# Optimization experiments

Hardware: AMD Instinct MI355X
Metric: run time of the kernel (lower is better)

Reference implementation:

```python
import jax, jax.numpy as jnp
import numpy as np

N = 50000      # nodes
E = 800000     # edges
IN = 128       # in_dim
H = 128        # hidden_dim
OUT = 64       # out_dim
B = 6          # block_num
NEG_SLOPE = 0.01  # nn.LeakyReLU default


def setup_inputs() -> dict:
    key = jax.random.key(0)
    ks = jax.random.split(key, 10)
    s = 0.05
    return {
        "inputs": jax.random.normal(ks[0], (N, IN), jnp.float32),
        "edges": jax.random.randint(ks[1], (2, E), 0, N, jnp.int32),
        "w_in": jax.random.normal(ks[2], (IN, H), jnp.float32) * s,
        "b_in": jnp.zeros((H,), jnp.float32),
        "w1": jax.random.normal(ks[3], (B, H, H), jnp.float32) * s,
        "b1": jnp.zeros((B, H), jnp.float32),
        "w2": jax.random.normal(ks[4], (B, H, H), jnp.float32) * s,
        "b2": jnp.zeros((B, H), jnp.float32),
        "w_out": jax.random.normal(ks[5], (H, OUT), jnp.float32) * s,
        "b_out": jnp.zeros((OUT,), jnp.float32),
    }


def _leaky(x):
    return jnp.where(x >= 0, x, NEG_SLOPE * x)


def _gcn_conv(x, W, b, src, dst, norm):
    # GCNConv: out = D^{-1/2}(A+I)D^{-1/2} (x W) + b, with self-loops folded in.
    xw = x @ W                                   # [N, d_out]
    msg = xw[src] * norm[src, None]              # gather + edge scaling [E, d_out]
    agg = jax.ops.segment_sum(msg, dst, num_segments=N)
    agg = agg * norm[:, None] + xw * (norm * norm)[:, None]  # neighbors + self-loop
    return agg + b


def reference(inputs, edges, w_in, b_in, w1, b1, w2, b2, w_out, b_out):
    src, dst = edges[0], edges[1]
    deg = 1.0 + jax.ops.segment_sum(jnp.ones((E,), inputs.dtype), dst, num_segments=N)
    norm = jax.lax.rsqrt(deg)                    # [N]

    x = _leaky(_gcn_conv(inputs, w_in, b_in, src, dst, norm))
    for i in range(B):  # fixed small layer loop (structurally distinct params)
        h = _leaky(_gcn_conv(x, w1[i], b1[i], src, dst, norm))
        h = _leaky(_gcn_conv(h, w2[i], b2[i], src, dst, norm))
        x = (x + h) * 0.5
    # dropout in eval mode -> identity
    x_out = _gcn_conv(x, w_out, b_out, src, dst, norm)
    return (x_out, x)
```

## Files before the change

### kernel.cpp

```cpp
#include <hip/hip_runtime.h>

#define NNODES 50000
#define NPAD   50048
#define NEDGES 800000
#define HDIM 128
#define OUTDIM 64

#define GEMM_GRID 391
#define GEMM_BLK  512
#define GEMM_TILES (NPAD / 16)

typedef short short8 __attribute__((ext_vector_type(8)));
typedef _Float16 half8 __attribute__((ext_vector_type(8)));
typedef _Float16 half4 __attribute__((ext_vector_type(4)));
typedef float f32x4 __attribute__((ext_vector_type(4)));
typedef float f32x8 __attribute__((ext_vector_type(8)));

__device__ __forceinline__ unsigned short f2bf(float f) {
    unsigned int u = __builtin_bit_cast(unsigned int, f);
    unsigned int r = (u + 0x7FFFu + ((u >> 16) & 1u)) >> 16;
    return (unsigned short)r;
}
__device__ __forceinline__ float bf2f(unsigned short b) {
    unsigned int u = ((unsigned int)b) << 16;
    return __builtin_bit_cast(float, u);
}

__global__ void count_kernel(const int* __restrict__ dst, int* __restrict__ deg,
                             int* __restrict__ epos) {
    int e = blockIdx.x * 256 + threadIdx.x;
    if (e < NEDGES) epos[e] = atomicAdd(&deg[dst[e]], 1);
}

__global__ __launch_bounds__(256) void bsum_kernel(const int* __restrict__ deg,
                                                   int* __restrict__ bsum) {
    __shared__ int red[256];
    int i = blockIdx.x * 256 + threadIdx.x;
    red[threadIdx.x] = (i < NNODES) ? deg[i] : 0;
    __syncthreads();
    for (int off = 128; off; off >>= 1) {
        if (threadIdx.x < off) red[threadIdx.x] += red[threadIdx.x + off];
        __syncthreads();
    }
    if (threadIdx.x == 0) bsum[blockIdx.x] = red[0];
}

__global__ __launch_bounds__(256) void bscan_kernel(const int* __restrict__ bsum,
                                                    int* __restrict__ bofs) {
    __shared__ int s[256];
    int t = threadIdx.x;
    int v = (t < 196) ? bsum[t] : 0;
    s[t] = v;
    __syncthreads();
    for (int off = 1; off < 256; off <<= 1) {
        int u = (t >= off) ? s[t - off] : 0;
        __syncthreads();
        s[t] += u;
        __syncthreads();
    }
    if (t < 196) bofs[t] = s[t] - v;
}

__global__ __launch_bounds__(256) void emit_kernel(
    const int* __restrict__ deg, const int* __restrict__ bofs,
    int* __restrict__ row_ptr, float* __restrict__ norm) {
    __shared__ int s[256];
    int t = threadIdx.x;
    int i = blockIdx.x * 256 + t;
    int v = (i < NNODES) ? deg[i] : 0;
    s[t] = v;
    __syncthreads();
    for (int off = 1; off < 256; off <<= 1) {
        int u = (t >= off) ? s[t - off] : 0;
        __syncthreads();
        s[t] += u;
        __syncthreads();
    }
    int excl = s[t] - v + bofs[blockIdx.x];
    if (i < NNODES) {
        row_ptr[i] = excl;
        norm[i] = rsqrtf(1.0f + (float)v);
    }
    if (i == NNODES - 1) row_ptr[NNODES] = NEDGES;
}

__global__ void fill_kernel(const int* __restrict__ src, const int* __restrict__ dst,
                            const int* __restrict__ epos, const int* __restrict__ row_ptr,
                            int* __restrict__ sorted_src) {
    int e = blockIdx.x * 256 + threadIdx.x;
    if (e < NEDGES) sorted_src[row_ptr[dst[e]] + epos[e]] = src[e];
}

__global__ __launch_bounds__(256) void prep_w_kernel(
    const float* __restrict__ w_in, const float* __restrict__ w1,
    const float* __restrict__ w2, const float* __restrict__ w_out,
    unsigned short* __restrict__ wT, _Float16* __restrict__ w2f) {
    int idx = blockIdx.x * 256 + threadIdx.x;
    if (idx < 16384 + 98304) {
        const float* W;
        unsigned short* o;
        int e;
        if (idx < 16384) {
            W = w_in; o = wT; e = idx;
        } else {
            int j = idx - 16384; int m = j >> 14; e = j & 16383;
            W = w1 + ((size_t)m << 14); o = wT + (size_t)(1 + m) * 32768;
        }
        int k = e >> 7, n = e & 127;
        float v = W[e];
        unsigned short h = f2bf(v);
        o[(size_t)n * 256 + k] = h;
        o[(size_t)n * 256 + 128 + k] = f2bf(v - bf2f(h));
    } else if (idx < 16384 + 196608) {
        int j = idx - 16384 - 98304; int m = j >> 14; int e = j & 16383;
        int k = e >> 7, n = e & 127;
        w2f[(size_t)m * 16384 + n * 128 + k] = (_Float16)w2[((size_t)m << 14) + e];
    } else {
        int e = idx - 212992;
        int k = e >> 6, n = e & 63;
        float v = w_out[e];
        unsigned short h = f2bf(v);
        unsigned short* o = wT + (size_t)7 * 32768;
        o[(size_t)n * 256 + k] = h;
        o[(size_t)n * 256 + 128 + k] = f2bf(v - bf2f(h));
    }
}

__global__ __launch_bounds__(256) void split_x_kernel(
    const float* __restrict__ x, unsigned short* __restrict__ xc) {
    int gid = blockIdx.x * 256 + threadIdx.x;
    int row = gid >> 6;
    int kk = (gid & 63) * 2;
    float2 v = {0.f, 0.f};
    if (row < NNODES) v = *(const float2*)(x + (size_t)row * 128 + kk);
    unsigned short h0 = f2bf(v.x), h1 = f2bf(v.y);
    unsigned short l0 = f2bf(v.x - bf2f(h0)), l1 = f2bf(v.y - bf2f(h1));
    *(unsigned int*)(xc + (size_t)row * 256 + kk) =
        (unsigned int)h0 | ((unsigned int)h1 << 16);
    *(unsigned int*)(xc + (size_t)row * 256 + 128 + kk) =
        (unsigned int)l0 | ((unsigned int)l1 << 16);
}

template <int NCOLS>
__global__ __launch_bounds__(GEMM_BLK) void gemm_bf_kernel(
    const unsigned short* __restrict__ xc, const unsigned short* __restrict__ wT,
    const float* __restrict__ norm, _Float16* __restrict__ y) {
    __shared__ unsigned short Blds[NCOLS * 256];
    const int t = threadIdx.x;
    const int wave = t >> 6, lane = t & 63, quad = lane >> 4, l16 = lane & 15;

    constexpr int NCH = NCOLS * 32;
#pragma unroll
    for (int i = 0; i < NCH / GEMM_BLK; ++i) {
        int C = i * GEMM_BLK + t;
        int n = C >> 5, c = C & 31;
        const unsigned short* gp = wT + ((size_t)n << 8) + ((c ^ (n & 7)) << 3);
        unsigned short* lp = Blds + ((size_t)C << 3);
        __builtin_amdgcn_global_load_lds(
            (const __attribute__((address_space(1))) void*)gp,
            (__attribute__((address_space(3))) void*)lp, 16, 0, 0);
    }
    __syncthreads();

    const int wid = blockIdx.x * (GEMM_BLK / 64) + wave;
    const int sw = l16 & 7;
    const int rb0 = wid * 16;

    short8 a0[8];
    const unsigned short* ap0 = xc + ((size_t)(rb0 + l16) << 8) + quad * 8;
#pragma unroll
    for (int ck = 0; ck < 8; ++ck) a0[ck] = *(const short8*)(ap0 + ck * 32);

    float nm0[4];
#pragma unroll
    for (int r = 0; r < 4; ++r) {
        int r0 = rb0 + quad * 4 + r;
        nm0[r] = norm[r0 < NNODES ? r0 : 0];
    }

#pragma unroll
    for (int nt = 0; nt < NCOLS / 16; ++nt) {
        const unsigned short* bp = Blds + ((size_t)(nt * 16 + l16) << 8);
        short8 bh[4], bl[4];
#pragma unroll
        for (int ck = 0; ck < 4; ++ck) {
            bh[ck] = *(const short8*)(bp + (((ck * 4 + quad) ^ sw) << 3));
            bl[ck] = *(const short8*)(bp + (((16 + ck * 4 + quad) ^ sw) << 3));
        }
        f32x4 ac0 = (f32x4){0.f, 0.f, 0.f, 0.f};
#pragma unroll
        for (int ck = 0; ck < 4; ++ck) {
            ac0 = __builtin_amdgcn_mfma_f32_16x16x32_bf16(a0[ck], bh[ck], ac0, 0, 0, 0);
            ac0 = __builtin_amdgcn_mfma_f32_16x16x32_bf16(a0[ck], bl[ck], ac0, 0, 0, 0);
            ac0 = __builtin_amdgcn_mfma_f32_16x16x32_bf16(a0[4 + ck], bh[ck], ac0, 0, 0, 0);
        }
        int col = nt * 16 + l16;
#pragma unroll
        for (int r = 0; r < 4; ++r) {
            int r0 = rb0 + quad * 4 + r;
            if (r0 < NNODES) y[(size_t)r0 * NCOLS + col] = (_Float16)(ac0[r] * nm0[r]);
        }
    }
}

__global__ __launch_bounds__(GEMM_BLK) void gemm_f16_kernel(
    const _Float16* __restrict__ A, const _Float16* __restrict__ wf,
    const float* __restrict__ norm, _Float16* __restrict__ y) {
    __shared__ _Float16 Blds[128 * 128];
    const int t = threadIdx.x;
    const int wave = t >> 6, lane = t & 63, quad = lane >> 4, l16 = lane & 15;

#pragma unroll
    for (int i = 0; i < 2048 / GEMM_BLK; ++i) {
        int C = i * GEMM_BLK + t;
        int n = C >> 4, c = C & 15;
        const _Float16* gp = wf + ((size_t)n << 7) + ((c ^ (n & 7)) << 3);
        _Float16* lp = Blds + ((size_t)C << 3);
        __builtin_amdgcn_global_load_lds(
            (const __attribute__((address_space(1))) void*)gp,
            (__attribute__((address_space(3))) void*)lp, 16, 0, 0);
    }
    __syncthreads();

    const int wid = blockIdx.x * (GEMM_BLK / 64) + wave;
    const int sw = l16 & 7;
    const int rb0 = wid * 16;

    half8 a0[4];
    const _Float16* ap0 = A + ((size_t)(rb0 + l16) << 7) + quad * 8;
#pragma unroll
    for (int ck = 0; ck < 4; ++ck) a0[ck] = *(const half8*)(ap0 + ck * 32);

    float nm0[4];
#pragma unroll
    for (int r = 0; r < 4; ++r) {
        int r0 = rb0 + quad * 4 + r;
        nm0[r] = norm[r0 < NNODES ? r0 : 0];
    }

#pragma unroll
    for (int nt = 0; nt < 8; ++nt) {
        const _Float16* bp = Blds + ((size_t)(nt * 16 + l16) << 7);
        half8 b[4];
#pragma unroll
        for (int ck = 0; ck < 4; ++ck)
            b[ck] = *(const half8*)(bp + (((ck * 4 + quad) ^ sw) << 3));
        f32x4 ac0 = (f32x4){0.f, 0.f, 0.f, 0.f};
#pragma unroll
        for (int ck = 0; ck < 4; ++ck)
            ac0 = __builtin_amdgcn_mfma_f32_16x16x32_f16(a0[ck], b[ck], ac0, 0, 0, 0);
        int col = nt * 16 + l16;
#pragma unroll
        for (int r = 0; r < 4; ++r) {
            int r0 = rb0 + quad * 4 + r;
            if (r0 < NNODES) y[(size_t)r0 * 128 + col] = (_Float16)(ac0[r] * nm0[r]);
        }
    }
}

template <int MODE, bool WOUT, bool OUT16>
__global__ __launch_bounds__(256) void gather_fin128(
    const _Float16* __restrict__ y, const int* __restrict__ row_ptr,
    const int* __restrict__ sorted_src, const float* __restrict__ norm,
    const float* __restrict__ bias, const unsigned short* __restrict__ xcres,
    float* __restrict__ out, unsigned short* __restrict__ xcout,
    _Float16* __restrict__ h16) {
    const int wave = threadIdx.x >> 6;
    const int lane = threadIdx.x & 63;
    const int g = lane >> 4, j = lane & 15;
    const int n = blockIdx.x * 16 + wave * 4 + g;
    const int beg = row_ptr[n];
    const int deg = row_ptr[n + 1] - beg;
    int dmax = deg;
    dmax = max(dmax, __shfl_xor(dmax, 16));
    dmax = max(dmax, __shfl_xor(dmax, 32));

    f32x8 acc = (f32x8){0.f, 0.f, 0.f, 0.f, 0.f, 0.f, 0.f, 0.f};

    for (int i = 0; i < dmax; i += 8) {
        int sarr[8];
#pragma unroll
        for (int u = 0; u < 8; ++u)
            sarr[u] = (i + u < deg) ? sorted_src[beg + i + u] : -1;
        half8 h[8];
#pragma unroll
        for (int u = 0; u < 8; ++u)
            if (sarr[u] >= 0)
                h[u] = *(const half8*)(y + ((size_t)sarr[u] << 7) + j * 8);
#pragma unroll
        for (int u = 0; u < 8; ++u)
            if (sarr[u] >= 0) acc += __builtin_convertvector(h[u], f32x8);
    }

    const half8 sh = *(const half8*)(y + ((size_t)n << 7) + j * 8);
    const f32x4 b0 = *(const f32x4*)(bias + j * 8);
    const f32x4 b1 = *(const f32x4*)(bias + j * 8 + 4);
    const float bb[8] = {b0[0], b0[1], b0[2], b0[3], b1[0], b1[1], b1[2], b1[3]};
    const float nm = norm[n];
    float v[8];
#pragma unroll
    for (int c = 0; c < 8; ++c) {
        float t = (acc[c] + (float)sh[c]) * nm + bb[c];
        v[c] = t >= 0.f ? t : 0.01f * t;
    }
    if (MODE == 1) {
        short8 hw = __builtin_nontemporal_load(
            (const short8*)(xcres + ((size_t)n << 8) + j * 8));
        short8 lw = __builtin_nontemporal_load(
            (const short8*)(xcres + ((size_t)n << 8) + 128 + j * 8));
#pragma unroll
        for (int c = 0; c < 8; ++c) {
            float xr = bf2f((unsigned short)hw[c]) + bf2f((unsigned short)lw[c]);
            v[c] = (xr + v[c]) * 0.5f;
        }
    }
    if (WOUT) {
        f32x4 o0 = (f32x4){v[0], v[1], v[2], v[3]};
        f32x4 o1 = (f32x4){v[4], v[5], v[6], v[7]};
        __builtin_nontemporal_store(o0, (f32x4*)(out + ((size_t)n << 7) + j * 8));
        __builtin_nontemporal_store(o1, (f32x4*)(out + ((size_t)n << 7) + j * 8 + 4));
    }
    if (OUT16) {
        half8 o;
#pragma unroll
        for (int c = 0; c < 8; ++c) o[c] = (_Float16)v[c];
        *(half8*)(h16 + ((size_t)n << 7) + j * 8) = o;
    } else {
        short8 hi, lo;
#pragma unroll
        for (int c = 0; c < 8; ++c) {
            unsigned short hv = f2bf(v[c]);
            hi[c] = (short)hv;
            lo[c] = (short)f2bf(v[c] - bf2f(hv));
        }
        *(short8*)(xcout + ((size_t)n << 8) + j * 8) = hi;
        *(short8*)(xcout + ((size_t)n << 8) + 128 + j * 8) = lo;
    }
}

__global__ __launch_bounds__(256) void gather_fin64(
    const _Float16* __restrict__ y, const int* __restrict__ row_ptr,
    const int* __restrict__ sorted_src, const float* __restrict__ norm,
    const float* __restrict__ bias, float* __restrict__ out) {
    const int wave = threadIdx.x >> 6;
    const int lane = threadIdx.x & 63;
    const int g = lane >> 4, j = lane & 15;
    const int n = blockIdx.x * 16 + wave * 4 + g;
    const int beg = row_ptr[n];
    const int deg = row_ptr[n + 1] - beg;
    int dmax = deg;
    dmax = max(dmax, __shfl_xor(dmax, 16));
    dmax = max(dmax, __shfl_xor(dmax, 32));

    f32x4 acc = (f32x4){0.f, 0.f, 0.f, 0.f};
    for (int i = 0; i < dmax; i += 8) {
        int sarr[8];
#pragma unroll
        for (int u = 0; u < 8; ++u)
            sarr[u] = (i + u < deg) ? sorted_src[beg + i + u] : -1;
        half4 h[8];
#pragma unroll
        for (int u = 0; u < 8; ++u)
            if (sarr[u] >= 0)
                h[u] = *(const half4*)(y + ((size_t)sarr[u] << 6) + j * 4);
#pragma unroll
        for (int u = 0; u < 8; ++u)
            if (sarr[u] >= 0) acc += __builtin_convertvector(h[u], f32x4);
    }

    const half4 sh = *(const half4*)(y + ((size_t)n << 6) + j * 4);
    const f32x4 b = *(const f32x4*)(bias + j * 4);
    const float nm = norm[n];
    f32x4 o;
    o[0] = (acc[0] + (float)sh[0]) * nm + b[0];
    o[1] = (acc[1] + (float)sh[1]) * nm + b[1];
    o[2] = (acc[2] + (float)sh[2]) * nm + b[2];
    o[3] = (acc[3] + (float)sh[3]) * nm + b[3];
    __builtin_nontemporal_store(o, (f32x4*)(out + ((size_t)n << 6) + j * 4));
}

extern "C" void kernel_launch(void* const* d_in, const int* in_sizes, int n_in,
                              void* d_out, int out_size, void* d_ws, size_t ws_size,
                              hipStream_t stream) {
    const float* inputs = (const float*)d_in[0];
    const int* edges = (const int*)d_in[1];
    const int* src = edges;
    const int* dst = edges + NEDGES;
    const float* w_in  = (const float*)d_in[2];
    const float* b_in  = (const float*)d_in[3];
    const float* w1    = (const float*)d_in[4];
    const float* b1    = (const float*)d_in[5];
    const float* w2    = (const float*)d_in[6];
    const float* b2    = (const float*)d_in[7];
    const float* w_out = (const float*)d_in[8];
    const float* b_out = (const float*)d_in[9];

    float* out  = (float*)d_out;
    float* xout = out;
    float* x    = out + (size_t)NNODES * OUTDIM;

    char* p = (char*)d_ws;
    auto alloc = [&](size_t bytes) {
        char* r = p;
        p += (bytes + 63) & ~(size_t)63;
        return r;
    };
    int* deg        = (int*)alloc(NNODES * 4);
    int* epos       = (int*)alloc(NEDGES * 4);
    int* row_ptr    = (int*)alloc((NNODES + 1) * 4);
    int* bsum       = (int*)alloc(256 * 4);
    int* bofs       = (int*)alloc(256 * 4);
    int* sorted_src = (int*)alloc(NEDGES * 4);
    float* normb    = (float*)alloc(NNODES * 4);
    unsigned short* wT = (unsigned short*)alloc((size_t)245760 * 2);
    _Float16* w2f   = (_Float16*)alloc((size_t)6 * 16384 * 2);
    unsigned short* xc_x = (unsigned short*)alloc((size_t)NPAD * 256 * 2);
    unsigned short* xc_in = (unsigned short*)alloc((size_t)NPAD * 256 * 2);
    _Float16* h16   = (_Float16*)alloc((size_t)NPAD * 128 * 2);
    _Float16* y     = (_Float16*)alloc((size_t)NNODES * HDIM * 2);

    hipMemsetAsync(deg, 0, NNODES * sizeof(int), stream);
    count_kernel<<<(NEDGES + 255) / 256, 256, 0, stream>>>(dst, deg, epos);
    bsum_kernel<<<196, 256, 0, stream>>>(deg, bsum);
    bscan_kernel<<<1, 256, 0, stream>>>(bsum, bofs);
    emit_kernel<<<196, 256, 0, stream>>>(deg, bofs, row_ptr, normb);
    fill_kernel<<<(NEDGES + 255) / 256, 256, 0, stream>>>(src, dst, epos, row_ptr, sorted_src);
    prep_w_kernel<<<864, 256, 0, stream>>>(w_in, w1, w2, w_out, wT, w2f);

    split_x_kernel<<<(NPAD * 64) / 256, 256, 0, stream>>>(inputs, xc_in);
    gemm_bf_kernel<128><<<GEMM_GRID, GEMM_BLK, 0, stream>>>(xc_in, wT, normb, y);
    gather_fin128<0, false, false><<<NNODES / 16, 256, 0, stream>>>(
        y, row_ptr, sorted_src, normb, b_in, nullptr, nullptr, xc_x, nullptr);

    for (int i = 0; i < 6; ++i) {
        gemm_bf_kernel<128><<<GEMM_GRID, GEMM_BLK, 0, stream>>>(
            xc_x, wT + (size_t)(1 + i) * 32768, normb, y);
        gather_fin128<0, false, true><<<NNODES / 16, 256, 0, stream>>>(
            y, row_ptr, sorted_src, normb, b1 + i * HDIM, nullptr, nullptr, nullptr, h16);
        gemm_f16_kernel<<<GEMM_GRID, GEMM_BLK, 0, stream>>>(
            h16, w2f + (size_t)i * 16384, normb, y);
        if (i < 5)
            gather_fin128<1, false, false><<<NNODES / 16, 256, 0, stream>>>(
                y, row_ptr, sorted_src, normb, b2 + i * HDIM, xc_x, nullptr, xc_x, nullptr);
        else
            gather_fin128<1, true, false><<<NNODES / 16, 256, 0, stream>>>(
                y, row_ptr, sorted_src, normb, b2 + i * HDIM, xc_x, x, xc_x, nullptr);
    }

    gemm_bf_kernel<64><<<GEMM_GRID, GEMM_BLK, 0, stream>>>(
        xc_x, wT + (size_t)7 * 32768, normb, y);
    gather_fin64<<<NNODES / 16, 256, 0, stream>>>(
        y, row_ptr, sorted_src, normb, b_out, xout);
}
```

Before: 784.4 us.

## Fuse first-conv gather/finalize into second GEMM via LDS staging

Merges the gather-aggregate-finalize kernel of the first block conv into the following f16 GEMM. Each wave gathers neighbor rows for its 16 nodes, applies norm, bias and LeakyReLU, and stages the f16 result in LDS as the MFMA A operand. This removes the h16 round trip through global memory and one kernel launch per block, and writes the GEMM output to a separate buffer y2 so it does not overwrite y while other blocks still read it. In exchange, gather parallelism is reduced (391 blocks of 512 threads instead of 3125 blocks), LDS use grows by 32KB per block, and the gather latency now serializes ahead of the MFMA work.

Result: faster. 742.6 us (-5.3%).

```diff
diff --git a/kernel.cpp b/kernel.cpp
--- a/kernel.cpp
+++ b/kernel.cpp
@@ -203,10 +203,13 @@
     }
 }
 
-__global__ __launch_bounds__(GEMM_BLK) void gemm_f16_kernel(
-    const _Float16* __restrict__ A, const _Float16* __restrict__ wf,
-    const float* __restrict__ norm, _Float16* __restrict__ y) {
+__global__ __launch_bounds__(GEMM_BLK) void fgg_f16_kernel(
+    const _Float16* __restrict__ y, const int* __restrict__ row_ptr,
+    const int* __restrict__ sorted_src, const float* __restrict__ norm,
+    const float* __restrict__ bias, const _Float16* __restrict__ wf,
+    _Float16* __restrict__ yout) {
     __shared__ _Float16 Blds[128 * 128];
+    __shared__ _Float16 Alds[8 * 16 * 128];
     const int t = threadIdx.x;
     const int wave = t >> 6, lane = t & 63, quad = lane >> 4, l16 = lane & 15;
 
@@ -220,16 +223,63 @@
             (const __attribute__((address_space(1))) void*)gp,
             (__attribute__((address_space(3))) void*)lp, 16, 0, 0);
     }
+
+    const int wid = blockIdx.x * (GEMM_BLK / 64) + wave;
+    const int rb0 = wid * 16;
+    _Float16* Aw = Alds + (size_t)wave * 2048;
+    const int g = quad, j = l16;
+
+    for (int tb = 0; tb < 4; ++tb) {
+        const int n = rb0 + tb * 4 + g;
+        const bool valid = n < NNODES;
+        const int beg = valid ? row_ptr[n] : 0;
+        const int dg = valid ? (row_ptr[n + 1] - beg) : 0;
+        int dmax = dg;
+        dmax = max(dmax, __shfl_xor(dmax, 16));
+        dmax = max(dmax, __shfl_xor(dmax, 32));
+
+        f32x8 acc = (f32x8){0.f, 0.f, 0.f, 0.f, 0.f, 0.f, 0.f, 0.f};
+        for (int i = 0; i < dmax; i += 8) {
+            int sarr[8];
+#pragma unroll
+            for (int u = 0; u < 8; ++u)
+                sarr[u] = (i + u < dg) ? sorted_src[beg + i + u] : -1;
+            half8 h[8];
+#pragma unroll
+            for (int u = 0; u < 8; ++u)
+                if (sarr[u] >= 0)
+                    h[u] = *(const half8*)(y + ((size_t)sarr[u] << 7) + j * 8);
+#pragma unroll
+            for (int u = 0; u < 8; ++u)
+                if (sarr[u] >= 0) acc += __builtin_convertvector(h[u], f32x8);
+        }
+
+        half8 o;
+        if (valid) {
+            const half8 sh = *(const half8*)(y + ((size_t)n << 7) + j * 8);
+            const f32x4 b0 = *(const f32x4*)(bias + j * 8);
+            const f32x4 b1 = *(const f32x4*)(bias + j * 8 + 4);
+            const float bb[8] = {b0[0], b0[1], b0[2], b0[3], b1[0], b1[1], b1[2], b1[3]};
+            const float nm = norm[n];
+#pragma unroll
+            for (int c = 0; c < 8; ++c) {
+                float v = (acc[c] + (float)sh[c]) * nm + bb[c];
+                v = v >= 0.f ? v : 0.01f * v;
+                o[c] = (_Float16)v;
+            }
+        } else {
+#pragma unroll
+            for (int c = 0; c < 8; ++c) o[c] = (_Float16)0.f;
+        }
+        *(half8*)(Aw + (size_t)(tb * 4 + g) * 128 + j * 8) = o;
+    }
     __syncthreads();
 
-    const int wid = blockIdx.x * (GEMM_BLK / 64) + wave;
     const int sw = l16 & 7;
-    const int rb0 = wid * 16;
-
     half8 a0[4];
-    const _Float16* ap0 = A + ((size_t)(rb0 + l16) << 7) + quad * 8;
-#pragma unroll
-    for (int ck = 0; ck < 4; ++ck) a0[ck] = *(const half8*)(ap0 + ck * 32);
+#pragma unroll
+    for (int ck = 0; ck < 4; ++ck)
+        a0[ck] = *(const half8*)(Aw + (size_t)l16 * 128 + ck * 32 + quad * 8);
 
     float nm0[4];
 #pragma unroll
@@ -253,7 +303,7 @@
 #pragma unroll
         for (int r = 0; r < 4; ++r) {
             int r0 = rb0 + quad * 4 + r;
-            if (r0 < NNODES) y[(size_t)r0 * 128 + col] = (_Float16)(ac0[r] * nm0[r]);
+            if (r0 < NNODES) yout[(size_t)r0 * 128 + col] = (_Float16)(ac0[r] * nm0[r]);
         }
     }
 }
@@ -416,7 +466,7 @@
     _Float16* w2f   = (_Float16*)alloc((size_t)6 * 16384 * 2);
     unsigned short* xc_x = (unsigned short*)alloc((size_t)NPAD * 256 * 2);
     unsigned short* xc_in = (unsigned short*)alloc((size_t)NPAD * 256 * 2);
-    _Float16* h16   = (_Float16*)alloc((size_t)NPAD * 128 * 2);
+    _Float16* y2    = (_Float16*)alloc((size_t)NPAD * 128 * 2);
     _Float16* y     = (_Float16*)alloc((size_t)NNODES * HDIM * 2);
 
     hipMemsetAsync(deg, 0, NNODES * sizeof(int), stream);
@@ -435,16 +485,15 @@
     for (int i = 0; i < 6; ++i) {
         gemm_bf_kernel<128><<<GEMM_GRID, GEMM_BLK, 0, stream>>>(
             xc_x, wT + (size_t)(1 + i) * 32768, normb, y);
-        gather_fin128<0, false, true><<<NNODES / 16, 256, 0, stream>>>(
-            y, row_ptr, sorted_src, normb, b1 + i * HDIM, nullptr, nullptr, nullptr, h16);
-        gemm_f16_kernel<<<GEMM_GRID, GEMM_BLK, 0, stream>>>(
-            h16, w2f + (size_t)i * 16384, normb, y);
+        fgg_f16_kernel<<<GEMM_GRID, GEMM_BLK, 0, stream>>>(
+            y, row_ptr, sorted_src, normb, b1 + i * HDIM,
+            w2f + (size_t)i * 16384, y2);
         if (i < 5)
             gather_fin128<1, false, false><<<NNODES / 16, 256, 0, stream>>>(
-                y, row_ptr, sorted_src, normb, b2 + i * HDIM, xc_x, nullptr, xc_x, nullptr);
+                y2, row_ptr, sorted_src, normb, b2 + i * HDIM, xc_x, nullptr, xc_x, nullptr);
         else
             gather_fin128<1, true, false><<<NNODES / 16, 256, 0, stream>>>(
-                y, row_ptr, sorted_src, normb, b2 + i * HDIM, xc_x, x, xc_x, nullptr);
+                y2, row_ptr, sorted_src, normb, b2 + i * HDIM, xc_x, x, xc_x, nullptr);
     }
 
     gemm_bf_kernel<64><<<GEMM_GRID, GEMM_BLK, 0, stream>>>(
```

## Fuse gather-aggregate epilogue with next layer's GEMM and use f16 weights

Applied to the files above, without the earlier changes.

Each gather/finalize step now feeds its output rows straight into LDS and runs the following layer's f16 MFMA GEMM in the same kernel, removing the intermediate activation round trip and roughly halving kernel launches. The w1 and w_out GEMMs switch from split-bf16 (three MFMAs per step) to single f16 MFMAs, cutting GEMM work but lowering precision. Ping-pong y buffers are used so no kernel reads a buffer it is writing. The gather part now runs with 512-thread blocks across 391 blocks, which changes occupancy and latency hiding for the irregular gather.

Result: faster. 706.6 us (-9.9%).

```diff
diff --git a/kernel.cpp b/kernel.cpp
--- a/kernel.cpp
+++ b/kernel.cpp
@@ -8,7 +8,6 @@
 
 #define GEMM_GRID 391
 #define GEMM_BLK  512
-#define GEMM_TILES (NPAD / 16)
 
 typedef short short8 __attribute__((ext_vector_type(8)));
 typedef _Float16 half8 __attribute__((ext_vector_type(8)));
@@ -94,23 +93,20 @@
 __global__ __launch_bounds__(256) void prep_w_kernel(
     const float* __restrict__ w_in, const float* __restrict__ w1,
     const float* __restrict__ w2, const float* __restrict__ w_out,
-    unsigned short* __restrict__ wT, _Float16* __restrict__ w2f) {
+    unsigned short* __restrict__ wT, _Float16* __restrict__ w1f,
+    _Float16* __restrict__ w2f, _Float16* __restrict__ woutf) {
     int idx = blockIdx.x * 256 + threadIdx.x;
-    if (idx < 16384 + 98304) {
-        const float* W;
-        unsigned short* o;
-        int e;
-        if (idx < 16384) {
-            W = w_in; o = wT; e = idx;
-        } else {
-            int j = idx - 16384; int m = j >> 14; e = j & 16383;
-            W = w1 + ((size_t)m << 14); o = wT + (size_t)(1 + m) * 32768;
-        }
+    if (idx < 16384) {
+        int e = idx;
         int k = e >> 7, n = e & 127;
-        float v = W[e];
+        float v = w_in[e];
         unsigned short h = f2bf(v);
-        o[(size_t)n * 256 + k] = h;
-        o[(size_t)n * 256 + 128 + k] = f2bf(v - bf2f(h));
+        wT[(size_t)n * 256 + k] = h;
+        wT[(size_t)n * 256 + 128 + k] = f2bf(v - bf2f(h));
+    } else if (idx < 16384 + 98304) {
+        int j = idx - 16384; int m = j >> 14; int e = j & 16383;
+        int k = e >> 7, n = e & 127;
+        w1f[(size_t)m * 16384 + n * 128 + k] = (_Float16)w1[((size_t)m << 14) + e];
     } else if (idx < 16384 + 196608) {
         int j = idx - 16384 - 98304; int m = j >> 14; int e = j & 16383;
         int k = e >> 7, n = e & 127;
@@ -118,11 +114,7 @@
     } else {
         int e = idx - 212992;
         int k = e >> 6, n = e & 63;
-        float v = w_out[e];
-        unsigned short h = f2bf(v);
-        unsigned short* o = wT + (size_t)7 * 32768;
-        o[(size_t)n * 256 + k] = h;
-        o[(size_t)n * 256 + 128 + k] = f2bf(v - bf2f(h));
+        woutf[(size_t)n * 128 + k] = (_Float16)w_out[e];
     }
 }
 
@@ -203,15 +195,20 @@
     }
 }
 
-__global__ __launch_bounds__(GEMM_BLK) void gemm_f16_kernel(
-    const _Float16* __restrict__ A, const _Float16* __restrict__ wf,
-    const float* __restrict__ norm, _Float16* __restrict__ y) {
-    __shared__ _Float16 Blds[128 * 128];
+template <int MODE, int NCOLS, bool WRXC, bool WOUT>
+__global__ __launch_bounds__(GEMM_BLK) void fga_kernel(
+    const _Float16* __restrict__ y, const int* __restrict__ row_ptr,
+    const int* __restrict__ sorted_src, const float* __restrict__ norm,
+    const float* __restrict__ bias, const unsigned short* __restrict__ xcres,
+    const _Float16* __restrict__ wf, unsigned short* __restrict__ xcout,
+    float* __restrict__ xfull, _Float16* __restrict__ yout) {
+    __shared__ _Float16 Blds[NCOLS * 128];
+    __shared__ _Float16 Alds[8 * 16 * 128];
     const int t = threadIdx.x;
     const int wave = t >> 6, lane = t & 63, quad = lane >> 4, l16 = lane & 15;
 
 #pragma unroll
-    for (int i = 0; i < 2048 / GEMM_BLK; ++i) {
+    for (int i = 0; i < (NCOLS * 16) / GEMM_BLK; ++i) {
         int C = i * GEMM_BLK + t;
         int n = C >> 4, c = C & 15;
         const _Float16* gp = wf + ((size_t)n << 7) + ((c ^ (n & 7)) << 3);
@@ -223,13 +220,90 @@
     __syncthreads();
 
     const int wid = blockIdx.x * (GEMM_BLK / 64) + wave;
+    const int rb0 = wid * 16;
+    _Float16* Aw = Alds + (size_t)wave * 2048;
+    const int g = quad, j = l16;
+
+    for (int tb = 0; tb < 4; ++tb) {
+        const int n = rb0 + tb * 4 + g;
+        const bool valid = n < NNODES;
+        const int beg = valid ? row_ptr[n] : 0;
+        const int dg = valid ? (row_ptr[n + 1] - beg) : 0;
+        int dmax = dg;
+        dmax = max(dmax, __shfl_xor(dmax, 16));
+        dmax = max(dmax, __shfl_xor(dmax, 32));
+
+        f32x8 acc = (f32x8){0.f, 0.f, 0.f, 0.f, 0.f, 0.f, 0.f, 0.f};
+        for (int i = 0; i < dmax; i += 8) {
+            int sarr[8];
+#pragma unroll
+            for (int u = 0; u < 8; ++u)
+                sarr[u] = (i + u < dg) ? sorted_src[beg + i + u] : -1;
+            half8 h[8];
+#pragma unroll
+            for (int u = 0; u < 8; ++u)
+                if (sarr[u] >= 0)
+                    h[u] = *(const half8*)(y + ((size_t)sarr[u] << 7) + j * 8);
+#pragma unroll
+            for (int u = 0; u < 8; ++u)
+                if (sarr[u] >= 0) acc += __builtin_convertvector(h[u], f32x8);
+        }
+
+        half8 o;
+        if (valid) {
+            const half8 sh = *(const half8*)(y + ((size_t)n << 7) + j * 8);
+            const f32x4 b0 = *(const f32x4*)(bias + j * 8);
+            const f32x4 b1 = *(const f32x4*)(bias + j * 8 + 4);
+            const float bb[8] = {b0[0], b0[1], b0[2], b0[3], b1[0], b1[1], b1[2], b1[3]};
+            const float nm = norm[n];
+            float v[8];
+#pragma unroll
+            for (int c = 0; c < 8; ++c) {
+                float tv = (acc[c] + (float)sh[c]) * nm + bb[c];
+                v[c] = tv >= 0.f ? tv : 0.01f * tv;
+            }
+            if (MODE == 1) {
+                short8 hw = __builtin_nontemporal_load(
+                    (const short8*)(xcres + ((size_t)n << 8) + j * 8));
+                short8 lw = __builtin_nontemporal_load(
+                    (const short8*)(xcres + ((size_t)n << 8) + 128 + j * 8));
+#pragma unroll
+                for (int c = 0; c < 8; ++c) {
+                    float xr = bf2f((unsigned short)hw[c]) + bf2f((unsigned short)lw[c]);
+                    v[c] = (xr + v[c]) * 0.5f;
+                }
+            }
+            if (WOUT) {
+                f32x4 o0 = (f32x4){v[0], v[1], v[2], v[3]};
+                f32x4 o1 = (f32x4){v[4], v[5], v[6], v[7]};
+                __builtin_nontemporal_store(o0, (f32x4*)(xfull + ((size_t)n << 7) + j * 8));
+                __builtin_nontemporal_store(o1, (f32x4*)(xfull + ((size_t)n << 7) + j * 8 + 4));
+            }
+            if (WRXC) {
+                short8 hi, lo;
+#pragma unroll
+                for (int c = 0; c < 8; ++c) {
+                    unsigned short hv = f2bf(v[c]);
+                    hi[c] = (short)hv;
+                    lo[c] = (short)f2bf(v[c] - bf2f(hv));
+                }
+                *(short8*)(xcout + ((size_t)n << 8) + j * 8) = hi;
+                *(short8*)(xcout + ((size_t)n << 8) + 128 + j * 8) = lo;
+            }
+#pragma unroll
+            for (int c = 0; c < 8; ++c) o[c] = (_Float16)v[c];
+        } else {
+#pragma unroll
+            for (int c = 0; c < 8; ++c) o[c] = (_Float16)0.f;
+        }
+        *(half8*)(Aw + (size_t)(tb * 4 + g) * 128 + j * 8) = o;
+    }
+
     const int sw = l16 & 7;
-    const int rb0 = wid * 16;
-
     half8 a0[4];
-    const _Float16* ap0 = A + ((size_t)(rb0 + l16) << 7) + quad * 8;
-#pragma unroll
-    for (int ck = 0; ck < 4; ++ck) a0[ck] = *(const half8*)(ap0 + ck * 32);
+#pragma unroll
+    for (int ck = 0; ck < 4; ++ck)
+        a0[ck] = *(const half8*)(Aw + (size_t)l16 * 128 + ck * 32 + quad * 8);
 
     float nm0[4];
 #pragma unroll
@@ -239,7 +313,7 @@
     }
 
 #pragma unroll
-    for (int nt = 0; nt < 8; ++nt) {
+    for (int nt = 0; nt < NCOLS / 16; ++nt) {
         const _Float16* bp = Blds + ((size_t)(nt * 16 + l16) << 7);
         half8 b[4];
 #pragma unroll
@@ -253,88 +327,8 @@
 #pragma unroll
         for (int r = 0; r < 4; ++r) {
             int r0 = rb0 + quad * 4 + r;
-            if (r0 < NNODES) y[(size_t)r0 * 128 + col] = (_Float16)(ac0[r] * nm0[r]);
-        }
-    }
-}
-
-template <int MODE, bool WOUT, bool OUT16>
-__global__ __launch_bounds__(256) void gather_fin128(
-    const _Float16* __restrict__ y, const int* __restrict__ row_ptr,
-    const int* __restrict__ sorted_src, const float* __restrict__ norm,
-    const float* __restrict__ bias, const unsigned short* __restrict__ xcres,
-    float* __restrict__ out, unsigned short* __restrict__ xcout,
-    _Float16* __restrict__ h16) {
-    const int wave = threadIdx.x >> 6;
-    const int lane = threadIdx.x & 63;
-    const int g = lane >> 4, j = lane & 15;
-    const int n = blockIdx.x * 16 + wave * 4 + g;
-    const int beg = row_ptr[n];
-    const int deg = row_ptr[n + 1] - beg;
-    int dmax = deg;
-    dmax = max(dmax, __shfl_xor(dmax, 16));
-    dmax = max(dmax, __shfl_xor(dmax, 32));
-
-    f32x8 acc = (f32x8){0.f, 0.f, 0.f, 0.f, 0.f, 0.f, 0.f, 0.f};
-
-    for (int i = 0; i < dmax; i += 8) {
-        int sarr[8];
-#pragma unroll
-        for (int u = 0; u < 8; ++u)
-            sarr[u] = (i + u < deg) ? sorted_src[beg + i + u] : -1;
-        half8 h[8];
-#pragma unroll
-        for (int u = 0; u < 8; ++u)
-            if (sarr[u] >= 0)
-                h[u] = *(const half8*)(y + ((size_t)sarr[u] << 7) + j * 8);
-#pragma unroll
-        for (int u = 0; u < 8; ++u)
-            if (sarr[u] >= 0) acc += __builtin_convertvector(h[u], f32x8);
-    }
-
-    const half8 sh = *(const half8*)(y + ((size_t)n << 7) + j * 8);
-    const f32x4 b0 = *(const f32x4*)(bias + j * 8);
-    const f32x4 b1 = *(const f32x4*)(bias + j * 8 + 4);
-    const float bb[8] = {b0[0], b0[1], b0[2], b0[3], b1[0], b1[1], b1[2], b1[3]};
-    const float nm = norm[n];
-    float v[8];
-#pragma unroll
-    for (int c = 0; c < 8; ++c) {
-        float t = (acc[c] + (float)sh[c]) * nm + bb[c];
-        v[c] = t >= 0.f ? t : 0.01f * t;
-    }
-    if (MODE == 1) {
-        short8 hw = __builtin_nontemporal_load(
-            (const short8*)(xcres + ((size_t)n << 8) + j * 8));
-        short8 lw = __builtin_nontemporal_load(
-            (const short8*)(xcres + ((size_t)n << 8) + 128 + j * 8));
-#pragma unroll
-        for (int c = 0; c < 8; ++c) {
-            float xr = bf2f((unsigned short)hw[c]) + bf2f((unsigned short)lw[c]);
-            v[c] = (xr + v[c]) * 0.5f;
-        }
-    }
-    if (WOUT) {
-        f32x4 o0 = (f32x4){v[0], v[1], v[2], v[3]};
-        f32x4 o1 = (f32x4){v[4], v[5], v[6], v[7]};
-        __builtin_nontemporal_store(o0, (f32x4*)(out + ((size_t)n << 7) + j * 8));
-        __builtin_nontemporal_store(o1, (f32x4*)(out + ((size_t)n << 7) + j * 8 + 4));
-    }
-    if (OUT16) {
-        half8 o;
-#pragma unroll
-        for (int c = 0; c < 8; ++c) o[c] = (_Float16)v[c];
-        *(half8*)(h16 + ((size_t)n << 7) + j * 8) = o;
-    } else {
-        short8 hi, lo;
-#pragma unroll
-        for (int c = 0; c < 8; ++c) {
-            unsigned short hv = f2bf(v[c]);
-            hi[c] = (short)hv;
-            lo[c] = (short)f2bf(v[c] - bf2f(hv));
-        }
-        *(short8*)(xcout + ((size_t)n << 8) + j * 8) = hi;
-        *(short8*)(xcout + ((size_t)n << 8) + 128 + j * 8) = lo;
+            if (r0 < NNODES) yout[(size_t)r0 * NCOLS + col] = (_Float16)(ac0[r] * nm0[r]);
+        }
     }
 }
 
@@ -412,12 +406,14 @@
     int* bofs       = (int*)alloc(256 * 4);
     int* sorted_src = (int*)alloc(NEDGES * 4);
     float* normb    = (float*)alloc(NNODES * 4);
-    unsigned short* wT = (unsigned short*)alloc((size_t)245760 * 2);
+    unsigned short* wT = (unsigned short*)alloc((size_t)32768 * 2);
+    _Float16* w1f   = (_Float16*)alloc((size_t)6 * 16384 * 2);
     _Float16* w2f   = (_Float16*)alloc((size_t)6 * 16384 * 2);
+    _Float16* woutf = (_Float16*)alloc((size_t)8192 * 2);
     unsigned short* xc_x = (unsigned short*)alloc((size_t)NPAD * 256 * 2);
     unsigned short* xc_in = (unsigned short*)alloc((size_t)NPAD * 256 * 2);
-    _Float16* h16   = (_Float16*)alloc((size_t)NPAD * 128 * 2);
-    _Float16* y     = (_Float16*)alloc((size_t)NNODES * HDIM * 2);
+    _Float16* yA    = (_Float16*)alloc((size_t)NPAD * 128 * 2);
+    _Float16* yB    = (_Float16*)alloc((size_t)NPAD * 128 * 2);
 
     hipMemsetAsync(deg, 0, NNODES * sizeof(int), stream);
     count_kernel<<<(NEDGES + 255) / 256, 256, 0, stream>>>(dst, deg, epos);
@@ -425,30 +421,28 @@
     bscan_kernel<<<1, 256, 0, stream>>>(bsum, bofs);
     emit_kernel<<<196, 256, 0, stream>>>(deg, bofs, row_ptr, normb);
     fill_kernel<<<(NEDGES + 255) / 256, 256, 0, stream>>>(src, dst, epos, row_ptr, sorted_src);
-    prep_w_kernel<<<864, 256, 0, stream>>>(w_in, w1, w2, w_out, wT, w2f);
+    prep_w_kernel<<<864, 256, 0, stream>>>(w_in, w1, w2, w_out, wT, w1f, w2f, woutf);
 
     split_x_kernel<<<(NPAD * 64) / 256, 256, 0, stream>>>(inputs, xc_in);
-    gemm_bf_kernel<128><<<GEMM_GRID, GEMM_BLK, 0, stream>>>(xc_in, wT, normb, y);
-    gather_fin128<0, false, false><<<NNODES / 16, 256, 0, stream>>>(
-        y, row_ptr, sorted_src, normb, b_in, nullptr, nullptr, xc_x, nullptr);
+    gemm_bf_kernel<128><<<GEMM_GRID, GEMM_BLK, 0, stream>>>(xc_in, wT, normb, yA);
+
+    fga_kernel<0, 128, true, false><<<GEMM_GRID, GEMM_BLK, 0, stream>>>(
+        yA, row_ptr, sorted_src, normb, b_in, nullptr, w1f, xc_x, nullptr, yB);
 
     for (int i = 0; i < 6; ++i) {
-        gemm_bf_kernel<128><<<GEMM_GRID, GEMM_BLK, 0, stream>>>(
-            xc_x, wT + (size_t)(1 + i) * 32768, normb, y);
-        gather_fin128<0, false, true><<<NNODES / 16, 256, 0, stream>>>(
-            y, row_ptr, sorted_src, normb, b1 + i * HDIM, nullptr, nullptr, nullptr, h16);
-        gemm_f16_kernel<<<GEMM_GRID, GEMM_BLK, 0, stream>>>(
-            h16, w2f + (size_t)i * 16384, normb, y);
+        fga_kernel<0, 128, false, false><<<GEMM_GRID, GEMM_BLK, 0, stream>>>(
+            yB, row_ptr, sorted_src, normb, b1 + i * HDIM, nullptr,
+            w2f + (size_t)i * 16384, nullptr, nullptr, yA);
         if (i < 5)
-            gather_fin128<1, false, false><<<NNODES / 16, 256, 0, stream>>>(
-                y, row_ptr, sorted_src, normb, b2 + i * HDIM, xc_x, nullptr, xc_x, nullptr);
+            fga_kernel<1, 128, true, false><<<GEMM_GRID, GEMM_BLK, 0, stream>>>(
+                yA, row_ptr, sorted_src, normb, b2 + i * HDIM, xc_x,
+                w1f + (size_t)(i + 1) * 16384, xc_x, nullptr, yB);
         else
-            gather_fin128<1, true, false><<<NNODES / 16, 256, 0, stream>>>(
-                y, row_ptr, sorted_src, normb, b2 + i * HDIM, xc_x, x, xc_x, nullptr);
-    }
-
-    gemm_bf_kernel<64><<<GEMM_GRID, GEMM_BLK, 0, stream>>>(
-        xc_x, wT + (size_t)7 * 32768, normb, y);
+            fga_kernel<1, 64, false, true><<<GEMM_GRID, GEMM_BLK, 0, stream>>>(
+                yA, row_ptr, sorted_src, normb, b2 + i * HDIM, xc_x,
+                woutf, nullptr, x, yB);
+    }
+
     gather_fin64<<<NNODES / 16, 256, 0, stream>>>(
-        y, row_ptr, sorted_src, normb, b_out, xout);
-}
+        yB, row_ptr, sorted_src, normb, b_out, xout);
+}
```
